# Kernel tuning notes

Hardware: AMD Instinct MI355X
Metric: run time of the kernel (lower is better)

## Reference

```python
import jax, jax.numpy as jnp
import numpy as np

N, E, F_IN, EDGE_DIM = 100000, 1600000, 128, 16
HID, H1, NUM_CLASSES = 16, 8, 16
NEG_SLOPE = 0.2


def segment_softmax(logits, seg, num_segments):
    # logits: [E, H], seg: [E] destination node ids
    m = jax.ops.segment_max(logits, seg, num_segments=num_segments)
    m = jnp.where(jnp.isfinite(m), m, jnp.zeros_like(m))
    e = jnp.exp(logits - m[seg])
    s = jax.ops.segment_sum(e, seg, num_segments=num_segments)
    return e / (s[seg] + 1e-16)


def gat_layer(x, src, dst, edge_attr, W, att_s, att_d, We, att_e, bias, concat):
    n = x.shape[0]
    H, C = att_s.shape[1], att_s.shape[2]
    xh = (x @ W).reshape(n, H, C)                 # shared lin_src == lin_dst
    a_s = (xh * att_s).sum(-1)                    # [N, H]
    a_d = (xh * att_d).sum(-1)                    # [N, H]
    eh = (edge_attr @ We).reshape(-1, H, C)       # [E, H, C]
    a_e = (eh * att_e).sum(-1)                    # [E, H]
    alpha = a_s[src] + a_d[dst] + a_e             # alpha_j + alpha_i + alpha_edge
    alpha = jax.nn.leaky_relu(alpha, NEG_SLOPE)
    alpha = segment_softmax(alpha, dst, n)        # softmax keyed by dst index
    msg = xh[src] * alpha[..., None]              # [E, H, C]
    out = jax.ops.segment_sum(msg, dst, num_segments=n)  # [N, H, C]
    out = out.reshape(n, H * C) if concat else out.mean(axis=1)
    return out + bias


def setup_inputs() -> dict:
    key = jax.random.key(0)
    ks = jax.random.split(key, 16)
    glorot = lambda k, shape: jax.random.uniform(
        k, shape, jnp.float32, -1.0, 1.0) * np.sqrt(6.0 / (shape[-1] + shape[-2] if len(shape) > 1 else shape[-1]))
    x = jax.random.normal(ks[0], (N, F_IN), jnp.float32)
    edge_index = jax.random.randint(ks[1], (2, E), 0, N, jnp.int64)
    edge_attr = jax.random.normal(ks[2], (E, EDGE_DIM), jnp.float32)
    # layer 1: in=F_IN, out=HID, heads=H1, concat=True
    W1 = glorot(ks[3], (F_IN, H1 * HID))
    att_src1 = glorot(ks[4], (1, H1, HID))
    att_dst1 = glorot(ks[5], (1, H1, HID))
    We1 = glorot(ks[6], (EDGE_DIM, H1 * HID))
    att_edge1 = glorot(ks[7], (1, H1, HID))
    b1 = jnp.zeros((H1 * HID,), jnp.float32)
    # layer 2: in=H1*HID, out=NUM_CLASSES, heads=1, concat=False
    W2 = glorot(ks[8], (H1 * HID, 1 * NUM_CLASSES))
    att_src2 = glorot(ks[9], (1, 1, NUM_CLASSES))
    att_dst2 = glorot(ks[10], (1, 1, NUM_CLASSES))
    We2 = glorot(ks[11], (EDGE_DIM, 1 * NUM_CLASSES))
    att_edge2 = glorot(ks[12], (1, 1, NUM_CLASSES))
    b2 = jnp.zeros((NUM_CLASSES,), jnp.float32)
    return dict(x=x, edge_index=edge_index, edge_attr=edge_attr,
                W1=W1, att_src1=att_src1, att_dst1=att_dst1, We1=We1, att_edge1=att_edge1, b1=b1,
                W2=W2, att_src2=att_src2, att_dst2=att_dst2, We2=We2, att_edge2=att_edge2, b2=b2)


def reference(x, edge_index, edge_attr,
              W1, att_src1, att_dst1, We1, att_edge1, b1,
              W2, att_src2, att_dst2, We2, att_edge2, b2):
    src, dst = edge_index[0], edge_index[1]
    # eval mode: all dropout (p=0.6) layers are identity
    h = gat_layer(x, src, dst, edge_attr, W1, att_src1, att_dst1, We1, att_edge1, b1, concat=True)
    h = jax.nn.elu(h)
    h = gat_layer(h, src, dst, edge_attr, W2, att_src2, att_dst2, We2, att_edge2, b2, concat=False)
    return jax.nn.log_softmax(h, axis=1)
```

## Files before the change

kernel.cpp:

```cpp
#include <hip/hip_runtime.h>
#include <hip/hip_bf16.h>

#define N_NODES 100000
#define N_EDGES 1600000
#define NEG_SLOPE 0.2f
#define LDS_STRIDE 132

typedef __attribute__((ext_vector_type(8))) short short8;
typedef __attribute__((ext_vector_type(4))) short short4v;
typedef __attribute__((ext_vector_type(4))) float floatx4;

__device__ inline short f2bf(float f) {
    __hip_bfloat16 h = __float2bfloat16(f);
    return *reinterpret_cast<short*>(&h);
}
__device__ inline float bf2f(unsigned short u) {
    union { unsigned int i; float f; } z; z.i = ((unsigned int)u) << 16; return z.f;
}

__global__ void k_pre(const float* __restrict__ We1, const float* __restrict__ attE1,
                      const float* __restrict__ We2, const float* __restrict__ attE2,
                      float* __restrict__ M1, float* __restrict__ M2) {
    int t = threadIdx.x;
    if (t < 128) {
        int d = t >> 3, h = t & 7;
        float s = 0.f;
        for (int c = 0; c < 16; ++c) s += We1[d * 128 + h * 16 + c] * attE1[h * 16 + c];
        M1[d * 8 + h] = s;
    } else if (t < 144) {
        int d = t - 128;
        float s = 0.f;
        for (int c = 0; c < 16; ++c) s += We2[d * 16 + c] * attE2[c];
        M2[d] = s;
    }
}

__global__ __launch_bounds__(256) void k_gemm1(
    const float* __restrict__ x, const float* __restrict__ W1,
    const float* __restrict__ attS, const float* __restrict__ attD,
    __hip_bfloat16* __restrict__ xh1b, float* __restrict__ a1s, float* __restrict__ a1d) {
    __shared__ short lds[128 * LDS_STRIDE];
    int t = threadIdx.x;
    for (int i = t * 4; i < 16384; i += 1024) {
        float4 v = *(const float4*)(W1 + i);
        int k = i >> 7, n = i & 127;
        lds[(n + 0) * LDS_STRIDE + k] = f2bf(v.x);
        lds[(n + 1) * LDS_STRIDE + k] = f2bf(v.y);
        lds[(n + 2) * LDS_STRIDE + k] = f2bf(v.z);
        lds[(n + 3) * LDS_STRIDE + k] = f2bf(v.w);
    }
    __syncthreads();
    int w = t >> 6, l = t & 63;
    int q = l >> 4, m = l & 15;
    int row = blockIdx.x * 64 + w * 16 + m;
    int rowc = row < N_NODES ? row : 0;
    floatx4 acc[8];
#pragma unroll
    for (int nt = 0; nt < 8; ++nt) acc[nt] = (floatx4){0.f, 0.f, 0.f, 0.f};
#pragma unroll
    for (int KK = 0; KK < 4; ++KK) {
        int k0 = KK * 32 + q * 8;
        float4 alo = *(const float4*)(x + (size_t)rowc * 128 + k0);
        float4 ahi = *(const float4*)(x + (size_t)rowc * 128 + k0 + 4);
        short8 a = {f2bf(alo.x), f2bf(alo.y), f2bf(alo.z), f2bf(alo.w),
                    f2bf(ahi.x), f2bf(ahi.y), f2bf(ahi.z), f2bf(ahi.w)};
#pragma unroll
        for (int nt = 0; nt < 8; ++nt) {
            const short* bp = &lds[(nt * 16 + m) * LDS_STRIDE + k0];
            short4v blo = *(const short4v*)bp;
            short4v bhi = *(const short4v*)(bp + 4);
            short8 b = {blo.x, blo.y, blo.z, blo.w, bhi.x, bhi.y, bhi.z, bhi.w};
            acc[nt] = __builtin_amdgcn_mfma_f32_16x16x32_bf16(a, b, acc[nt], 0, 0, 0);
        }
    }
    int rb = blockIdx.x * 64 + w * 16 + q * 4;
#pragma unroll
    for (int nt = 0; nt < 8; ++nt) {
        float aS = attS[nt * 16 + m], aD = attD[nt * 16 + m];
        float p0 = acc[nt][0] * aS, p1 = acc[nt][1] * aS, p2 = acc[nt][2] * aS, p3 = acc[nt][3] * aS;
        float d0 = acc[nt][0] * aD, d1 = acc[nt][1] * aD, d2 = acc[nt][2] * aD, d3 = acc[nt][3] * aD;
        for (int dd = 1; dd < 16; dd <<= 1) {
            p0 += __shfl_xor(p0, dd); p1 += __shfl_xor(p1, dd);
            p2 += __shfl_xor(p2, dd); p3 += __shfl_xor(p3, dd);
            d0 += __shfl_xor(d0, dd); d1 += __shfl_xor(d1, dd);
            d2 += __shfl_xor(d2, dd); d3 += __shfl_xor(d3, dd);
        }
        if (m == 0) {
            if (rb + 0 < N_NODES) { a1s[(size_t)(rb+0)*8+nt] = p0; a1d[(size_t)(rb+0)*8+nt] = d0; }
            if (rb + 1 < N_NODES) { a1s[(size_t)(rb+1)*8+nt] = p1; a1d[(size_t)(rb+1)*8+nt] = d1; }
            if (rb + 2 < N_NODES) { a1s[(size_t)(rb+2)*8+nt] = p2; a1d[(size_t)(rb+2)*8+nt] = d2; }
            if (rb + 3 < N_NODES) { a1s[(size_t)(rb+3)*8+nt] = p3; a1d[(size_t)(rb+3)*8+nt] = d3; }
        }
    }
    __syncthreads();
#pragma unroll
    for (int nt = 0; nt < 8; ++nt) {
#pragma unroll
        for (int r = 0; r < 4; ++r)
            lds[(w * 16 + q * 4 + r) * LDS_STRIDE + nt * 16 + m] = f2bf(acc[nt][r]);
    }
    __syncthreads();
    int r2 = t >> 2, c2 = (t & 3) * 32;
    int gr = blockIdx.x * 64 + r2;
    if (gr < N_NODES) {
        short* gp = (short*)(xh1b + (size_t)gr * 128 + c2);
#pragma unroll
        for (int i = 0; i < 8; ++i)
            *(short4v*)(gp + i * 4) = *(const short4v*)&lds[r2 * LDS_STRIDE + c2 + i * 4];
    }
}

__global__ void k_hist(const int* __restrict__ dst, int* __restrict__ count) {
    int i = blockIdx.x * blockDim.x + threadIdx.x;
    if (i < N_EDGES) atomicAdd(&count[dst[i]], 1);
}

__global__ __launch_bounds__(256) void k_scan1(const int* __restrict__ count,
                                               int* __restrict__ offs, int* __restrict__ partials) {
    __shared__ int s[256];
    int t = threadIdx.x;
    int i = blockIdx.x * 256 + t;
    int v = (i < N_NODES) ? count[i] : 0;
    s[t] = v; __syncthreads();
    for (int off = 1; off < 256; off <<= 1) {
        int add = (t >= off) ? s[t - off] : 0;
        __syncthreads();
        s[t] += add; __syncthreads();
    }
    if (i < N_NODES) offs[i] = s[t] - v;
    if (t == 255) partials[blockIdx.x] = s[255];
}

__global__ __launch_bounds__(512) void k_scan2(int* __restrict__ partials, int nb) {
    __shared__ int s[512];
    int t = threadIdx.x;
    int v = (t < nb) ? partials[t] : 0;
    s[t] = v; __syncthreads();
    for (int off = 1; off < 512; off <<= 1) {
        int add = (t >= off) ? s[t - off] : 0;
        __syncthreads();
        s[t] += add; __syncthreads();
    }
    if (t < nb) partials[t] = s[t] - v;
}

__global__ void k_scan3(int* __restrict__ offs, const int* __restrict__ partials) {
    int i = blockIdx.x * 256 + threadIdx.x;
    if (i < N_NODES) offs[i] += partials[blockIdx.x];
}

__global__ __launch_bounds__(256) void k_scatter(
    const int* __restrict__ dst, const int* __restrict__ offs,
    int* __restrict__ cursor, int* __restrict__ eid) {
    int e = blockIdx.x * 256 + threadIdx.x;
    int d = dst[e];
    int p = offs[d] + atomicAdd(&cursor[d], 1);
    eid[p] = e;
}

__global__ __launch_bounds__(256) void k_attn(
    const int* __restrict__ eid, const int* __restrict__ src, const int* __restrict__ dst,
    const float* __restrict__ ea, const float* __restrict__ M1, const float* __restrict__ M2,
    const float* __restrict__ a1s, const float* __restrict__ a1d,
    float* __restrict__ ew1c, float* __restrict__ ae2c, int* __restrict__ srcc) {
    __shared__ float M1s[128], M2s[16];
    int t = threadIdx.x;
    if (t < 128) M1s[t] = M1[t];
    if (t >= 128 && t < 144) M2s[t - 128] = M2[t - 128];
    __syncthreads();
    int p = blockIdx.x * 256 + t;
    int e = eid[p];
    int s = src[e], d = dst[e];
    float eav[16];
#pragma unroll
    for (int qq = 0; qq < 4; ++qq) {
        float4 v = *(const float4*)(ea + (size_t)e * 16 + qq * 4);
        eav[qq * 4] = v.x; eav[qq * 4 + 1] = v.y; eav[qq * 4 + 2] = v.z; eav[qq * 4 + 3] = v.w;
    }
    float ae1[8];
#pragma unroll
    for (int h = 0; h < 8; ++h) ae1[h] = 0.f;
#pragma unroll
    for (int dd = 0; dd < 16; ++dd) {
#pragma unroll
        for (int h = 0; h < 8; ++h) ae1[h] += eav[dd] * M1s[dd * 8 + h];
    }
    float aes = 0.f;
#pragma unroll
    for (int dd = 0; dd < 16; ++dd) aes += eav[dd] * M2s[dd];
    float4 s0 = *(const float4*)(a1s + (size_t)s * 8);
    float4 s1 = *(const float4*)(a1s + (size_t)s * 8 + 4);
    float4 d0 = *(const float4*)(a1d + (size_t)d * 8);
    float4 d1 = *(const float4*)(a1d + (size_t)d * 8 + 4);
    float as_[8] = {s0.x, s0.y, s0.z, s0.w, s1.x, s1.y, s1.z, s1.w};
    float ad_[8] = {d0.x, d0.y, d0.z, d0.w, d1.x, d1.y, d1.z, d1.w};
    float ew[8];
#pragma unroll
    for (int h = 0; h < 8; ++h) {
        float v = as_[h] + ad_[h] + ae1[h];
        v = v > 0.f ? v : NEG_SLOPE * v;
        ew[h] = __expf(v);
    }
    float4 w0 = {ew[0], ew[1], ew[2], ew[3]};
    float4 w1 = {ew[4], ew[5], ew[6], ew[7]};
    *(float4*)(ew1c + (size_t)p * 8) = w0;
    *(float4*)(ew1c + (size_t)p * 8 + 4) = w1;
    ae2c[p] = aes;
    srcc[p] = s;
}

__global__ __launch_bounds__(128) void k_agg1(
    const int* __restrict__ srcc, const float* __restrict__ ew1c,
    const __hip_bfloat16* __restrict__ xh1b, const int* __restrict__ offs,
    const int* __restrict__ count, const float* __restrict__ b1, float* __restrict__ h1) {
    __shared__ float4 racc[32];
    __shared__ float rw[32];
    int n = blockIdx.x;
    int t = threadIdx.x;
    int j = t & 31, k = t >> 5;
    int start = offs[n], deg = count[n];
    float4 acc = {0.f, 0.f, 0.f, 0.f};
    float wsum = 0.f;
    int i = k;
    int s = 0; float w = 0.f;
    if (i < deg) {
        int p = start + i;
        s = srcc[p];
        w = ew1c[(size_t)p * 8 + (j >> 2)];
    }
    while (i < deg) {
        int ni = i + 4;
        int ns = 0; float nw = 0.f;
        if (ni < deg) {
            int np = start + ni;
            ns = srcc[np];
            nw = ew1c[(size_t)np * 8 + (j >> 2)];
        }
        uint2 xv = *(const uint2*)((const char*)xh1b + (size_t)s * 256 + j * 8);
        float x0 = bf2f((unsigned short)(xv.x & 0xffff));
        float x1 = bf2f((unsigned short)(xv.x >> 16));
        float x2 = bf2f((unsigned short)(xv.y & 0xffff));
        float x3 = bf2f((unsigned short)(xv.y >> 16));
        acc.x += w * x0; acc.y += w * x1; acc.z += w * x2; acc.w += w * x3;
        wsum += w;
        i = ni; s = ns; w = nw;
    }
    acc.x += __shfl_xor(acc.x, 32); acc.y += __shfl_xor(acc.y, 32);
    acc.z += __shfl_xor(acc.z, 32); acc.w += __shfl_xor(acc.w, 32);
    wsum += __shfl_xor(wsum, 32);
    if (t >= 64 && t < 96) { racc[j] = acc; rw[j] = wsum; }
    __syncthreads();
    if (t < 32) {
        float4 o = racc[j];
        acc.x += o.x; acc.y += o.y; acc.z += o.z; acc.w += o.w;
        wsum += rw[j];
        float inv = 1.f / (wsum + 1e-16f);
        float4 b = *(const float4*)(b1 + j * 4);
        float4 r;
        r.x = acc.x * inv + b.x; r.y = acc.y * inv + b.y;
        r.z = acc.z * inv + b.z; r.w = acc.w * inv + b.w;
        r.x = r.x > 0.f ? r.x : __expf(r.x) - 1.f;
        r.y = r.y > 0.f ? r.y : __expf(r.y) - 1.f;
        r.z = r.z > 0.f ? r.z : __expf(r.z) - 1.f;
        r.w = r.w > 0.f ? r.w : __expf(r.w) - 1.f;
        *(float4*)(h1 + (size_t)n * 128 + j * 4) = r;
    }
}

__global__ __launch_bounds__(256) void k_gemm2(
    const float* __restrict__ h1, const float* __restrict__ W2,
    const float* __restrict__ attS, const float* __restrict__ attD,
    float* __restrict__ xh2, float* __restrict__ a2s, float* __restrict__ a2d) {
    __shared__ float W2s[128 * 16];
    __shared__ float hs[16 * 132];
    int t = threadIdx.x;
    for (int i = t * 4; i < 2048; i += 1024)
        *(float4*)(W2s + i) = *(const float4*)(W2 + i);
    size_t base = (size_t)blockIdx.x * 16 * 128;
    for (int i = t * 4; i < 2048; i += 1024) {
        float4 v = *(const float4*)(h1 + base + i);
        int r = i >> 7, k = i & 127;
        float* dstp = hs + r * 132 + k;
        dstp[0] = v.x; dstp[1] = v.y; dstp[2] = v.z; dstp[3] = v.w;
    }
    __syncthreads();
    int r = t >> 4, c = t & 15;
    float acc = 0.f;
#pragma unroll 4
    for (int k = 0; k < 128; ++k) acc += hs[r * 132 + k] * W2s[k * 16 + c];
    int row = blockIdx.x * 16 + r;
    xh2[(size_t)row * 16 + c] = acc;
    float ps = acc * attS[c], pd = acc * attD[c];
#pragma unroll
    for (int m = 1; m < 16; m <<= 1) { ps += __shfl_xor(ps, m); pd += __shfl_xor(pd, m); }
    if (c == 0) { a2s[row] = ps; a2d[row] = pd; }
}

__global__ __launch_bounds__(64) void k_agg2(
    const int* __restrict__ srcc, const float* __restrict__ ae2c,
    const float* __restrict__ a2s, const float* __restrict__ a2d, const float* __restrict__ xh2,
    const int* __restrict__ offs, const int* __restrict__ count,
    const float* __restrict__ b2, float* __restrict__ out) {
    int n = blockIdx.x;
    int t = threadIdx.x;
    int l = t & 3, k = t >> 2;
    int start = offs[n], deg = count[n];
    float ad = a2d[n];
    float4 acc = {0.f, 0.f, 0.f, 0.f};
    float wsum = 0.f;
    for (int i = k; i < deg; i += 16) {
        int p = start + i;
        int s = srcc[p];
        float lg = a2s[s] + ad + ae2c[p];
        lg = lg > 0.f ? lg : NEG_SLOPE * lg;
        float w = __expf(lg);
        float4 xv = *(const float4*)(xh2 + (size_t)s * 16 + l * 4);
        acc.x += w * xv.x; acc.y += w * xv.y; acc.z += w * xv.z; acc.w += w * xv.w;
        wsum += w;
    }
#pragma unroll
    for (int m = 4; m < 64; m <<= 1) {
        acc.x += __shfl_xor(acc.x, m); acc.y += __shfl_xor(acc.y, m);
        acc.z += __shfl_xor(acc.z, m); acc.w += __shfl_xor(acc.w, m);
        wsum += __shfl_xor(wsum, m);
    }
    float inv = 1.f / (wsum + 1e-16f);
    float4 b = *(const float4*)(b2 + l * 4);
    float4 lo;
    lo.x = acc.x * inv + b.x; lo.y = acc.y * inv + b.y;
    lo.z = acc.z * inv + b.z; lo.w = acc.w * inv + b.w;
    float mx = fmaxf(fmaxf(lo.x, lo.y), fmaxf(lo.z, lo.w));
    mx = fmaxf(mx, __shfl_xor(mx, 1)); mx = fmaxf(mx, __shfl_xor(mx, 2));
    float ex = __expf(lo.x - mx) + __expf(lo.y - mx) + __expf(lo.z - mx) + __expf(lo.w - mx);
    ex += __shfl_xor(ex, 1); ex += __shfl_xor(ex, 2);
    float ls = mx + __logf(ex);
    if (t < 4) {
        float4 r = {lo.x - ls, lo.y - ls, lo.z - ls, lo.w - ls};
        *(float4*)(out + (size_t)n * 16 + l * 4) = r;
    }
}

extern "C" void kernel_launch(void* const* d_in, const int* in_sizes, int n_in,
                              void* d_out, int out_size, void* d_ws, size_t ws_size,
                              hipStream_t stream) {
    const float* x     = (const float*)d_in[0];
    const int*   ei    = (const int*)d_in[1];
    const float* ea    = (const float*)d_in[2];
    const float* W1    = (const float*)d_in[3];
    const float* attS1 = (const float*)d_in[4];
    const float* attD1 = (const float*)d_in[5];
    const float* We1   = (const float*)d_in[6];
    const float* attE1 = (const float*)d_in[7];
    const float* b1    = (const float*)d_in[8];
    const float* W2    = (const float*)d_in[9];
    const float* attS2 = (const float*)d_in[10];
    const float* attD2 = (const float*)d_in[11];
    const float* We2   = (const float*)d_in[12];
    const float* attE2 = (const float*)d_in[13];
    const float* b2    = (const float*)d_in[14];
    float* out = (float*)d_out;
    const int* src = ei;
    const int* dst = ei + N_EDGES;

    char* p = (char*)d_ws;
    auto alloc = [&](size_t bytes) { char* r = p; p += (bytes + 255) & ~(size_t)255; return r; };
    __hip_bfloat16* xh1b = (__hip_bfloat16*)alloc((size_t)N_NODES * 128 * 2);
    float* h1       = (float*)alloc((size_t)N_NODES * 128 * 4);
    float* ew1c     = (float*)alloc((size_t)N_EDGES * 8 * 4);
    float* ae2c     = (float*)alloc((size_t)N_EDGES * 4);
    int*   srcc     = (int*)alloc((size_t)N_EDGES * 4);
    float* xh2      = (float*)alloc((size_t)N_NODES * 16 * 4);
    float* a2s      = (float*)alloc((size_t)N_NODES * 4);
    float* a2d      = (float*)alloc((size_t)N_NODES * 4);
    float* a1s      = (float*)alloc((size_t)N_NODES * 8 * 4);
    float* a1d      = (float*)alloc((size_t)N_NODES * 8 * 4);
    int*   eid      = (int*)alloc((size_t)N_EDGES * 4);
    int*   count    = (int*)alloc((size_t)N_NODES * 4);
    int*   cursor   = (int*)alloc((size_t)N_NODES * 4);
    int*   offs     = (int*)alloc((size_t)(N_NODES + 1) * 4);
    int*   partials = (int*)alloc(1024 * 4);
    float* M1       = (float*)alloc(128 * 4);
    float* M2       = (float*)alloc(64 * 4);
    if ((size_t)(p - (char*)d_ws) > ws_size) return;

    const int nb_scan = (N_NODES + 255) / 256;

    hipMemsetAsync(count, 0, (size_t)2 * N_NODES * 4 + 256, stream);
    k_pre<<<1, 192, 0, stream>>>(We1, attE1, We2, attE2, M1, M2);
    k_gemm1<<<(N_NODES + 63) / 64, 256, 0, stream>>>(x, W1, attS1, attD1, xh1b, a1s, a1d);
    k_hist<<<(N_EDGES + 255) / 256, 256, 0, stream>>>(dst, count);
    k_scan1<<<nb_scan, 256, 0, stream>>>(count, offs, partials);
    k_scan2<<<1, 512, 0, stream>>>(partials, nb_scan);
    k_scan3<<<nb_scan, 256, 0, stream>>>(offs, partials);
    k_scatter<<<N_EDGES / 256, 256, 0, stream>>>(dst, offs, cursor, eid);
    k_attn<<<N_EDGES / 256, 256, 0, stream>>>(eid, src, dst, ea, M1, M2, a1s, a1d,
                                              ew1c, ae2c, srcc);
    k_agg1<<<N_NODES, 128, 0, stream>>>(srcc, ew1c, xh1b, offs, count, b1, h1);
    k_gemm2<<<N_NODES / 16, 256, 0, stream>>>(h1, W2, attS2, attD2, xh2, a2s, a2d);
    k_agg2<<<N_NODES, 64, 0, stream>>>(srcc, ae2c, a2s, a2d, xh2, offs, count, b2, out);
}
```

Measured before the change: 678.7 us.

## Pack edge ids with src/dst in scatter, tile gemm1 over more rows, unroll agg1

k_scatter now writes an int4 of (edge id, src, dst) into the CSR-ordered slot. This lets k_attn read its indices in one coalesced load instead of gathering src[e] and dst[e] through eid. k_gemm1 processes 128 rows per block with a separate output LDS buffer, which amortizes the W1 transpose/convert, and writes W as packed 32-bit pairs. k_agg1 issues two independent neighbor loads per iteration for more memory-level parallelism. The costs are 16-byte scattered writes in place of 4-byte ones, and higher LDS use per gemm1 block, which may reduce occupancy.

New measurement: 614.9 us. 1.1x faster.

```diff
diff --git a/kernel.cpp b/kernel.cpp
--- a/kernel.cpp
+++ b/kernel.cpp
@@ -39,74 +39,85 @@
     const float* __restrict__ x, const float* __restrict__ W1,
     const float* __restrict__ attS, const float* __restrict__ attD,
     __hip_bfloat16* __restrict__ xh1b, float* __restrict__ a1s, float* __restrict__ a1d) {
-    __shared__ short lds[128 * LDS_STRIDE];
-    int t = threadIdx.x;
-    for (int i = t * 4; i < 16384; i += 1024) {
-        float4 v = *(const float4*)(W1 + i);
-        int k = i >> 7, n = i & 127;
-        lds[(n + 0) * LDS_STRIDE + k] = f2bf(v.x);
-        lds[(n + 1) * LDS_STRIDE + k] = f2bf(v.y);
-        lds[(n + 2) * LDS_STRIDE + k] = f2bf(v.z);
-        lds[(n + 3) * LDS_STRIDE + k] = f2bf(v.w);
+    __shared__ short ldsW[128 * LDS_STRIDE];
+    __shared__ short ldsO[64 * LDS_STRIDE];
+    int t = threadIdx.x;
+    unsigned int* ldsW32 = (unsigned int*)ldsW;
+    for (int u = t; u < 2048; u += 256) {
+        int kp = u >> 5;
+        int n4 = (u & 31) * 4;
+        float4 a = *(const float4*)(W1 + (size_t)(2 * kp) * 128 + n4);
+        float4 b = *(const float4*)(W1 + (size_t)(2 * kp + 1) * 128 + n4);
+        ldsW32[(n4 + 0) * 66 + kp] =
+            (unsigned int)(unsigned short)f2bf(a.x) | ((unsigned int)(unsigned short)f2bf(b.x) << 16);
+        ldsW32[(n4 + 1) * 66 + kp] =
+            (unsigned int)(unsigned short)f2bf(a.y) | ((unsigned int)(unsigned short)f2bf(b.y) << 16);
+        ldsW32[(n4 + 2) * 66 + kp] =
+            (unsigned int)(unsigned short)f2bf(a.z) | ((unsigned int)(unsigned short)f2bf(b.z) << 16);
+        ldsW32[(n4 + 3) * 66 + kp] =
+            (unsigned int)(unsigned short)f2bf(a.w) | ((unsigned int)(unsigned short)f2bf(b.w) << 16);
     }
     __syncthreads();
     int w = t >> 6, l = t & 63;
     int q = l >> 4, m = l & 15;
-    int row = blockIdx.x * 64 + w * 16 + m;
-    int rowc = row < N_NODES ? row : 0;
-    floatx4 acc[8];
-#pragma unroll
-    for (int nt = 0; nt < 8; ++nt) acc[nt] = (floatx4){0.f, 0.f, 0.f, 0.f};
-#pragma unroll
-    for (int KK = 0; KK < 4; ++KK) {
-        int k0 = KK * 32 + q * 8;
-        float4 alo = *(const float4*)(x + (size_t)rowc * 128 + k0);
-        float4 ahi = *(const float4*)(x + (size_t)rowc * 128 + k0 + 4);
-        short8 a = {f2bf(alo.x), f2bf(alo.y), f2bf(alo.z), f2bf(alo.w),
-                    f2bf(ahi.x), f2bf(ahi.y), f2bf(ahi.z), f2bf(ahi.w)};
+#pragma unroll
+    for (int rt = 0; rt < 2; ++rt) {
+        int row = blockIdx.x * 128 + rt * 64 + w * 16 + m;
+        int rowc = row < N_NODES ? row : 0;
+        floatx4 acc[8];
+#pragma unroll
+        for (int nt = 0; nt < 8; ++nt) acc[nt] = (floatx4){0.f, 0.f, 0.f, 0.f};
+#pragma unroll
+        for (int KK = 0; KK < 4; ++KK) {
+            int k0 = KK * 32 + q * 8;
+            float4 alo = *(const float4*)(x + (size_t)rowc * 128 + k0);
+            float4 ahi = *(const float4*)(x + (size_t)rowc * 128 + k0 + 4);
+            short8 a = {f2bf(alo.x), f2bf(alo.y), f2bf(alo.z), f2bf(alo.w),
+                        f2bf(ahi.x), f2bf(ahi.y), f2bf(ahi.z), f2bf(ahi.w)};
+#pragma unroll
+            for (int nt = 0; nt < 8; ++nt) {
+                const short* bp = &ldsW[(nt * 16 + m) * LDS_STRIDE + k0];
+                short4v blo = *(const short4v*)bp;
+                short4v bhi = *(const short4v*)(bp + 4);
+                short8 b = {blo.x, blo.y, blo.z, blo.w, bhi.x, bhi.y, bhi.z, bhi.w};
+                acc[nt] = __builtin_amdgcn_mfma_f32_16x16x32_bf16(a, b, acc[nt], 0, 0, 0);
+            }
+        }
+        int rb = blockIdx.x * 128 + rt * 64 + w * 16 + q * 4;
 #pragma unroll
         for (int nt = 0; nt < 8; ++nt) {
-            const short* bp = &lds[(nt * 16 + m) * LDS_STRIDE + k0];
-            short4v blo = *(const short4v*)bp;
-            short4v bhi = *(const short4v*)(bp + 4);
-            short8 b = {blo.x, blo.y, blo.z, blo.w, bhi.x, bhi.y, bhi.z, bhi.w};
-            acc[nt] = __builtin_amdgcn_mfma_f32_16x16x32_bf16(a, b, acc[nt], 0, 0, 0);
+            float aS = attS[nt * 16 + m], aD = attD[nt * 16 + m];
+            float p0 = acc[nt][0] * aS, p1 = acc[nt][1] * aS, p2 = acc[nt][2] * aS, p3 = acc[nt][3] * aS;
+            float d0 = acc[nt][0] * aD, d1 = acc[nt][1] * aD, d2 = acc[nt][2] * aD, d3 = acc[nt][3] * aD;
+            for (int dd = 1; dd < 16; dd <<= 1) {
+                p0 += __shfl_xor(p0, dd); p1 += __shfl_xor(p1, dd);
+                p2 += __shfl_xor(p2, dd); p3 += __shfl_xor(p3, dd);
+                d0 += __shfl_xor(d0, dd); d1 += __shfl_xor(d1, dd);
+                d2 += __shfl_xor(d2, dd); d3 += __shfl_xor(d3, dd);
+            }
+            if (m == 0) {
+                if (rb + 0 < N_NODES) { a1s[(size_t)(rb+0)*8+nt] = p0; a1d[(size_t)(rb+0)*8+nt] = d0; }
+                if (rb + 1 < N_NODES) { a1s[(size_t)(rb+1)*8+nt] = p1; a1d[(size_t)(rb+1)*8+nt] = d1; }
+                if (rb + 2 < N_NODES) { a1s[(size_t)(rb+2)*8+nt] = p2; a1d[(size_t)(rb+2)*8+nt] = d2; }
+                if (rb + 3 < N_NODES) { a1s[(size_t)(rb+3)*8+nt] = p3; a1d[(size_t)(rb+3)*8+nt] = d3; }
+            }
         }
-    }
-    int rb = blockIdx.x * 64 + w * 16 + q * 4;
-#pragma unroll
-    for (int nt = 0; nt < 8; ++nt) {
-        float aS = attS[nt * 16 + m], aD = attD[nt * 16 + m];
-        float p0 = acc[nt][0] * aS, p1 = acc[nt][1] * aS, p2 = acc[nt][2] * aS, p3 = acc[nt][3] * aS;
-        float d0 = acc[nt][0] * aD, d1 = acc[nt][1] * aD, d2 = acc[nt][2] * aD, d3 = acc[nt][3] * aD;
-        for (int dd = 1; dd < 16; dd <<= 1) {
-            p0 += __shfl_xor(p0, dd); p1 += __shfl_xor(p1, dd);
-            p2 += __shfl_xor(p2, dd); p3 += __shfl_xor(p3, dd);
-            d0 += __shfl_xor(d0, dd); d1 += __shfl_xor(d1, dd);
-            d2 += __shfl_xor(d2, dd); d3 += __shfl_xor(d3, dd);
+#pragma unroll
+        for (int nt = 0; nt < 8; ++nt) {
+#pragma unroll
+            for (int r = 0; r < 4; ++r)
+                ldsO[(w * 16 + q * 4 + r) * LDS_STRIDE + nt * 16 + m] = f2bf(acc[nt][r]);
         }
-        if (m == 0) {
-            if (rb + 0 < N_NODES) { a1s[(size_t)(rb+0)*8+nt] = p0; a1d[(size_t)(rb+0)*8+nt] = d0; }
-            if (rb + 1 < N_NODES) { a1s[(size_t)(rb+1)*8+nt] = p1; a1d[(size_t)(rb+1)*8+nt] = d1; }
-            if (rb + 2 < N_NODES) { a1s[(size_t)(rb+2)*8+nt] = p2; a1d[(size_t)(rb+2)*8+nt] = d2; }
-            if (rb + 3 < N_NODES) { a1s[(size_t)(rb+3)*8+nt] = p3; a1d[(size_t)(rb+3)*8+nt] = d3; }
+        __syncthreads();
+        int r2 = t >> 2, c2 = (t & 3) * 32;
+        int gr = blockIdx.x * 128 + rt * 64 + r2;
+        if (gr < N_NODES) {
+            short* gp = (short*)(xh1b + (size_t)gr * 128 + c2);
+#pragma unroll
+            for (int i = 0; i < 8; ++i)
+                *(short4v*)(gp + i * 4) = *(const short4v*)&ldsO[r2 * LDS_STRIDE + c2 + i * 4];
         }
-    }
-    __syncthreads();
-#pragma unroll
-    for (int nt = 0; nt < 8; ++nt) {
-#pragma unroll
-        for (int r = 0; r < 4; ++r)
-            lds[(w * 16 + q * 4 + r) * LDS_STRIDE + nt * 16 + m] = f2bf(acc[nt][r]);
-    }
-    __syncthreads();
-    int r2 = t >> 2, c2 = (t & 3) * 32;
-    int gr = blockIdx.x * 64 + r2;
-    if (gr < N_NODES) {
-        short* gp = (short*)(xh1b + (size_t)gr * 128 + c2);
-#pragma unroll
-        for (int i = 0; i < 8; ++i)
-            *(short4v*)(gp + i * 4) = *(const short4v*)&lds[r2 * LDS_STRIDE + c2 + i * 4];
+        __syncthreads();
     }
 }
 
@@ -150,16 +161,18 @@
 }
 
 __global__ __launch_bounds__(256) void k_scatter(
-    const int* __restrict__ dst, const int* __restrict__ offs,
-    int* __restrict__ cursor, int* __restrict__ eid) {
+    const int* __restrict__ src, const int* __restrict__ dst, const int* __restrict__ offs,
+    int* __restrict__ cursor, int4* __restrict__ pes) {
     int e = blockIdx.x * 256 + threadIdx.x;
     int d = dst[e];
+    int s = src[e];
     int p = offs[d] + atomicAdd(&cursor[d], 1);
-    eid[p] = e;
+    int4 v; v.x = e; v.y = s; v.z = d; v.w = 0;
+    pes[p] = v;
 }
 
 __global__ __launch_bounds__(256) void k_attn(
-    const int* __restrict__ eid, const int* __restrict__ src, const int* __restrict__ dst,
+    const int4* __restrict__ pes,
     const float* __restrict__ ea, const float* __restrict__ M1, const float* __restrict__ M2,
     const float* __restrict__ a1s, const float* __restrict__ a1d,
     float* __restrict__ ew1c, float* __restrict__ ae2c, int* __restrict__ srcc) {
@@ -169,8 +182,8 @@
     if (t >= 128 && t < 144) M2s[t - 128] = M2[t - 128];
     __syncthreads();
     int p = blockIdx.x * 256 + t;
-    int e = eid[p];
-    int s = src[e], d = dst[e];
+    int4 es = pes[p];
+    int e = es.x, s = es.y, d = es.z;
     float eav[16];
 #pragma unroll
     for (int qq = 0; qq < 4; ++qq) {
@@ -218,32 +231,32 @@
     int n = blockIdx.x;
     int t = threadIdx.x;
     int j = t & 31, k = t >> 5;
+    int hh = j >> 2;
     int start = offs[n], deg = count[n];
     float4 acc = {0.f, 0.f, 0.f, 0.f};
     float wsum = 0.f;
-    int i = k;
-    int s = 0; float w = 0.f;
-    if (i < deg) {
-        int p = start + i;
-        s = srcc[p];
-        w = ew1c[(size_t)p * 8 + (j >> 2)];
-    }
-    while (i < deg) {
-        int ni = i + 4;
-        int ns = 0; float nw = 0.f;
-        if (ni < deg) {
-            int np = start + ni;
-            ns = srcc[np];
-            nw = ew1c[(size_t)np * 8 + (j >> 2)];
+    for (int i = k; i < deg; i += 8) {
+        int p0 = start + i;
+        int s0 = srcc[p0];
+        float w0 = ew1c[(size_t)p0 * 8 + hh];
+        int i1 = i + 4;
+        int s1 = 0; float w1 = 0.f;
+        if (i1 < deg) {
+            int p1 = start + i1;
+            s1 = srcc[p1];
+            w1 = ew1c[(size_t)p1 * 8 + hh];
         }
-        uint2 xv = *(const uint2*)((const char*)xh1b + (size_t)s * 256 + j * 8);
-        float x0 = bf2f((unsigned short)(xv.x & 0xffff));
-        float x1 = bf2f((unsigned short)(xv.x >> 16));
-        float x2 = bf2f((unsigned short)(xv.y & 0xffff));
-        float x3 = bf2f((unsigned short)(xv.y >> 16));
-        acc.x += w * x0; acc.y += w * x1; acc.z += w * x2; acc.w += w * x3;
-        wsum += w;
-        i = ni; s = ns; w = nw;
+        uint2 xv0 = *(const uint2*)((const char*)xh1b + (size_t)s0 * 256 + j * 8);
+        uint2 xv1 = *(const uint2*)((const char*)xh1b + (size_t)s1 * 256 + j * 8);
+        acc.x += w0 * bf2f((unsigned short)(xv0.x & 0xffff));
+        acc.y += w0 * bf2f((unsigned short)(xv0.x >> 16));
+        acc.z += w0 * bf2f((unsigned short)(xv0.y & 0xffff));
+        acc.w += w0 * bf2f((unsigned short)(xv0.y >> 16));
+        acc.x += w1 * bf2f((unsigned short)(xv1.x & 0xffff));
+        acc.y += w1 * bf2f((unsigned short)(xv1.x >> 16));
+        acc.z += w1 * bf2f((unsigned short)(xv1.y & 0xffff));
+        acc.w += w1 * bf2f((unsigned short)(xv1.y >> 16));
+        wsum += w0 + w1;
     }
     acc.x += __shfl_xor(acc.x, 32); acc.y += __shfl_xor(acc.y, 32);
     acc.z += __shfl_xor(acc.z, 32); acc.w += __shfl_xor(acc.w, 32);
@@ -369,12 +382,12 @@
     float* ew1c     = (float*)alloc((size_t)N_EDGES * 8 * 4);
     float* ae2c     = (float*)alloc((size_t)N_EDGES * 4);
     int*   srcc     = (int*)alloc((size_t)N_EDGES * 4);
+    int4*  pes      = (int4*)alloc((size_t)N_EDGES * 16);
     float* xh2      = (float*)alloc((size_t)N_NODES * 16 * 4);
     float* a2s      = (float*)alloc((size_t)N_NODES * 4);
     float* a2d      = (float*)alloc((size_t)N_NODES * 4);
     float* a1s      = (float*)alloc((size_t)N_NODES * 8 * 4);
     float* a1d      = (float*)alloc((size_t)N_NODES * 8 * 4);
-    int*   eid      = (int*)alloc((size_t)N_EDGES * 4);
     int*   count    = (int*)alloc((size_t)N_NODES * 4);
     int*   cursor   = (int*)alloc((size_t)N_NODES * 4);
     int*   offs     = (int*)alloc((size_t)(N_NODES + 1) * 4);
@@ -387,13 +400,13 @@
 
     hipMemsetAsync(count, 0, (size_t)2 * N_NODES * 4 + 256, stream);
     k_pre<<<1, 192, 0, stream>>>(We1, attE1, We2, attE2, M1, M2);
-    k_gemm1<<<(N_NODES + 63) / 64, 256, 0, stream>>>(x, W1, attS1, attD1, xh1b, a1s, a1d);
+    k_gemm1<<<(N_NODES + 127) / 128, 256, 0, stream>>>(x, W1, attS1, attD1, xh1b, a1s, a1d);
     k_hist<<<(N_EDGES + 255) / 256, 256, 0, stream>>>(dst, count);
     k_scan1<<<nb_scan, 256, 0, stream>>>(count, offs, partials);
     k_scan2<<<1, 512, 0, stream>>>(partials, nb_scan);
     k_scan3<<<nb_scan, 256, 0, stream>>>(offs, partials);
-    k_scatter<<<N_EDGES / 256, 256, 0, stream>>>(dst, offs, cursor, eid);
-    k_attn<<<N_EDGES / 256, 256, 0, stream>>>(eid, src, dst, ea, M1, M2, a1s, a1d,
+    k_scatter<<<N_EDGES / 256, 256, 0, stream>>>(src, dst, offs, cursor, pes);
+    k_attn<<<N_EDGES / 256, 256, 0, stream>>>(pes, ea, M1, M2, a1s, a1d,
                                               ew1c, ae2c, srcc);
     k_agg1<<<N_NODES, 128, 0, stream>>>(srcc, ew1c, xh1b, offs, count, b1, h1);
     k_gemm2<<<N_NODES / 16, 256, 0, stream>>>(h1, W2, attS2, attD2, xh2, a2s, a2d);
```
